# Kernel tuning notes

Hardware: AMD Instinct MI355X
Metric: run time of the kernel (lower is better)

Reference implementation:

```python
import jax, jax.numpy as jnp
import numpy as np

B, T, V, E_DIM, M_DIM, H = 32, 256, 10000, 300, 128, 256


def setup_inputs() -> dict:
    key = jax.random.key(0)
    ks = jax.random.split(key, 8)
    sc = 0.05
    words = jax.random.randint(ks[0], (B, T), 0, V)            # int token ids, 0 = pad
    midis = jax.random.normal(ks[1], (B, T, M_DIM), dtype=jnp.float32)
    E  = jax.random.normal(ks[2], (V, E_DIM), dtype=jnp.float32) * sc   # embedding table
    Wm = jax.random.normal(ks[3], (M_DIM, E_DIM), dtype=jnp.float32) * sc  # midi Dense
    bm = jnp.zeros((E_DIM,), jnp.float32)
    Wx = jax.random.normal(ks[4], (E_DIM, 3 * H), dtype=jnp.float32) * sc  # GRU input kernel [z|r|h]
    bx = jnp.zeros((3 * H,), jnp.float32)
    U  = jax.random.normal(ks[5], (H, 3 * H), dtype=jnp.float32) * sc      # GRU recurrent kernel
    bu = jnp.zeros((3 * H,), jnp.float32)                                  # recurrent bias (reset_after)
    Wo = jax.random.normal(ks[6], (H, V), dtype=jnp.float32) * sc          # output Dense
    bo = jnp.zeros((V,), jnp.float32)
    return {"words": words, "midis": midis, "E": E, "Wm": Wm, "bm": bm,
            "Wx": Wx, "bx": bx, "U": U, "bu": bu, "Wo": Wo, "bo": bo}


def _gru_masked(x, mask, Wx, bx, U, bu):
    """Keras GRU (reset_after=True) with mask carry-through. x: [B,T,E], mask: [B,T] bool."""
    gx = x @ Wx + bx                      # [B,T,3H] precomputed input gates
    gx_t = jnp.swapaxes(gx, 0, 1)         # [T,B,3H]
    m_t = mask.T                          # [T,B]
    h0 = jnp.zeros((x.shape[0], H), x.dtype)

    def step(h, inp):
        g, m = inp
        gh = h @ U + bu                   # [B,3H]
        xz, xr, xn = jnp.split(g, 3, axis=-1)
        hz, hr, hn = jnp.split(gh, 3, axis=-1)
        z = jax.nn.sigmoid(xz + hz)
        r = jax.nn.sigmoid(xr + hr)
        n = jnp.tanh(xn + r * hn)         # reset_after: r applied to recurrent projection
        h_new = z * h + (1.0 - z) * n
        h_new = jnp.where(m[:, None], h_new, h)  # masked step: carry state/output
        return h_new, h_new

    h_last, seq = jax.lax.scan(step, h0, (gx_t, m_t))
    return jnp.swapaxes(seq, 0, 1), h_last  # [B,T,H], [B,H]


def reference(words, midis, E, Wm, bm, Wx, bx, U, bu, Wo, bo):
    mask = words != 0                      # Embedding(mask_zero=True).compute_mask
    x = E[words] + (midis @ Wm + bm)       # [B,T,E] fused embedding + dense add
    seq, _ = _gru_masked(x, mask, Wx, bx, U, bu)
    return seq @ Wo + bo                   # [B,T,V] logits
```

## Files before the change

### kernel.cpp

```cpp
#include <hip/hip_runtime.h>
#include <hip/hip_fp16.h>

typedef unsigned short ushort_t;
typedef short bf16x8 __attribute__((ext_vector_type(8)));
typedef float f32x4 __attribute__((ext_vector_type(4)));
typedef _Float16 f16x8 __attribute__((ext_vector_type(8)));

#define B_SZ 32
#define T_SZ 256
#define V_SZ 10000
#define E_DIM 300
#define M_DIM 128
#define H_SZ 256

__device__ __forceinline__ ushort_t f2bf(float f) {
  unsigned u = __float_as_uint(f);
  unsigned r = u + 0x7fffu + ((u >> 16) & 1u);
  return (ushort_t)(r >> 16);
}

__global__ void k_cast_bf16(const float* __restrict__ in, ushort_t* __restrict__ out, int n) {
  int i = blockIdx.x * blockDim.x + threadIdx.x;
  if (i < n) out[i] = f2bf(in[i]);
}

template <int MODE>
__global__ void k_transpose_cast(const float* __restrict__ in, ushort_t* __restrict__ out,
                                 int R, int C, int Rp, int Cp) {
  __shared__ float tile[32][33];
  int c0 = blockIdx.x * 32, r0 = blockIdx.y * 32;
  int tx = threadIdx.x, ty = threadIdx.y;
#pragma unroll
  for (int i = 0; i < 32; i += 8) {
    int r = r0 + ty + i, c = c0 + tx;
    tile[ty + i][tx] = (r < R && c < C) ? in[(size_t)r * C + c] : 0.f;
  }
  __syncthreads();
#pragma unroll
  for (int i = 0; i < 32; i += 8) {
    int c = c0 + ty + i, r = r0 + tx;
    if (c < Cp && r < Rp) {
      float v = tile[tx][ty + i];
      if (MODE == 0) {
        out[(size_t)c * Rp + r] = f2bf(v);
      } else {
        __half h = __float2half(v);
        out[(size_t)c * Rp + r] = *(ushort_t*)&h;
      }
    }
  }
}

__global__ void k_xfuse(const float* __restrict__ xtmp, const float* __restrict__ E,
                        const int* __restrict__ words, ushort_t* __restrict__ xb) {
  int m = blockIdx.x;
  int kp = threadIdx.x;
  int w = words[m];
  float v = 0.f;
  if (kp < E_DIM) v = xtmp[(size_t)m * 320 + kp] + E[(size_t)w * E_DIM + kp];
  xb[(size_t)m * 320 + kp] = f2bf(v);
}

__global__ __launch_bounds__(256, 2) void k_gemm_bt(
    const ushort_t* __restrict__ A, const ushort_t* __restrict__ BT,
    const float* __restrict__ bias, float* __restrict__ C,
    int M, int K, int Nreal, int ldc) {
  __shared__ __align__(16) char smem[32768];
  char* As = smem;
  char* Bs = smem + 16384;
  const int tid = threadIdx.x;
  const int lane = tid & 63;
  const int w = tid >> 6;
  const int wr = w >> 1, wc = w & 1;
  const int m0 = blockIdx.x * 128;
  const int n0 = blockIdx.y * 128;

  f32x4 acc[4][4];
#pragma unroll
  for (int i = 0; i < 4; ++i)
#pragma unroll
    for (int j = 0; j < 4; ++j) acc[i][j] = (f32x4){0.f, 0.f, 0.f, 0.f};

  const int srow = tid >> 3;
  const int sc16 = tid & 7;

  for (int k0 = 0; k0 < K; k0 += 64) {
    __syncthreads();
#pragma unroll
    for (int it = 0; it < 4; ++it) {
      int row = srow + it * 32;
      int slot = sc16 ^ (row & 7);
      bf16x8 va = *(const bf16x8*)(A + (size_t)(m0 + row) * K + k0 + sc16 * 8);
      *(bf16x8*)(As + row * 128 + (slot << 4)) = va;
      bf16x8 vb = *(const bf16x8*)(BT + (size_t)(n0 + row) * K + k0 + sc16 * 8);
      *(bf16x8*)(Bs + row * 128 + (slot << 4)) = vb;
    }
    __syncthreads();

    bf16x8 af[4][2], bfr[4][2];
#pragma unroll
    for (int mi = 0; mi < 4; ++mi) {
      int r = wr * 64 + mi * 16 + (lane & 15);
#pragma unroll
      for (int kk = 0; kk < 2; ++kk) {
        int c16 = kk * 4 + (lane >> 4);
        af[mi][kk] = *(const bf16x8*)(As + r * 128 + ((c16 ^ (r & 7)) << 4));
      }
    }
#pragma unroll
    for (int ni = 0; ni < 4; ++ni) {
      int r = wc * 64 + ni * 16 + (lane & 15);
#pragma unroll
      for (int kk = 0; kk < 2; ++kk) {
        int c16 = kk * 4 + (lane >> 4);
        bfr[ni][kk] = *(const bf16x8*)(Bs + r * 128 + ((c16 ^ (r & 7)) << 4));
      }
    }
#pragma unroll
    for (int mi = 0; mi < 4; ++mi)
#pragma unroll
      for (int ni = 0; ni < 4; ++ni)
#pragma unroll
        for (int kk = 0; kk < 2; ++kk)
          acc[mi][ni] = __builtin_amdgcn_mfma_f32_16x16x32_bf16(af[mi][kk], bfr[ni][kk],
                                                                acc[mi][ni], 0, 0, 0);
  }

  const int rbase = m0 + wr * 64 + (lane >> 4) * 4;
  const int cbase = n0 + wc * 64 + (lane & 15);
#pragma unroll
  for (int ni = 0; ni < 4; ++ni) {
    int n = cbase + ni * 16;
    if (n < Nreal) {
      float bn = bias[n];
#pragma unroll
      for (int mi = 0; mi < 4; ++mi) {
#pragma unroll
        for (int rg = 0; rg < 4; ++rg) {
          int mrow = rbase + mi * 16 + rg;
          C[(size_t)mrow * ldc + n] = acc[mi][ni][rg] + bn;
        }
      }
    }
  }
}

__global__ __launch_bounds__(512, 2) void k_gru(
    const float* __restrict__ gx, const ushort_t* __restrict__ UT,
    const float* __restrict__ bu, const int* __restrict__ words,
    ushort_t* __restrict__ seqb) {
  const int b = blockIdx.x;
  const int tid = threadIdx.x;
  const int lane = tid & 63;
  const int w = tid >> 6;

  __shared__ __align__(16) _Float16 hlds[16 * 256];
  __shared__ float ghbuf[768];
  __shared__ int words_s[T_SZ];

  for (int i = tid; i < 16 * 256; i += 512) hlds[i] = (_Float16)0.f;
  if (tid < T_SZ) words_s[tid] = words[b * T_SZ + tid];

  f16x8 Ufrag[6][8];
  {
    const int n0 = w * 96;
    const ushort_t* src = UT + (size_t)(n0 + (lane & 15)) * 256 + (lane >> 4) * 8;
#pragma unroll
    for (int ni = 0; ni < 6; ++ni) {
#pragma unroll
      for (int kk = 0; kk < 8; ++kk)
        Ufrag[ni][kk] = *(const f16x8*)(src + (size_t)ni * 16 * 256 + kk * 32);
    }
  }
  float buz = 0.f, bur = 0.f, bun = 0.f;
  if (tid < H_SZ) {
    buz = bu[tid];
    bur = bu[H_SZ + tid];
    bun = bu[2 * H_SZ + tid];
  }
  __syncthreads();

  const float* gxp = gx + (size_t)b * T_SZ * 768;
  float gxz = 0.f, gxr = 0.f, gxn = 0.f;
  if (tid < H_SZ) {
    gxz = gxp[tid];
    gxr = gxp[H_SZ + tid];
    gxn = gxp[2 * H_SZ + tid];
  }
  float h_old = 0.f;

  const int arow = lane & 15;
  const int abase = arow * 512;
  const int asub = lane >> 4;
  const int aswz = arow & 7;

  for (int t = 0; t < T_SZ; ++t) {
    float gxz_n = 0.f, gxr_n = 0.f, gxn_n = 0.f;
    if (t + 1 < T_SZ && tid < H_SZ) {
      const float* g1 = gxp + (size_t)(t + 1) * 768;
      gxz_n = g1[tid];
      gxr_n = g1[H_SZ + tid];
      gxn_n = g1[2 * H_SZ + tid];
    }

    f32x4 acc[6];
#pragma unroll
    for (int ni = 0; ni < 6; ++ni) acc[ni] = (f32x4){0.f, 0.f, 0.f, 0.f};
#pragma unroll
    for (int kk = 0; kk < 8; ++kk) {
      int c = kk * 4 + asub;
      f16x8 afrag = *(const f16x8*)((const char*)hlds + abase + ((c ^ aswz) << 4));
#pragma unroll
      for (int ni = 0; ni < 6; ++ni)
        acc[ni] = __builtin_amdgcn_mfma_f32_16x16x32_f16(afrag, Ufrag[ni][kk], acc[ni], 0, 0, 0);
    }
    if (lane < 16) {
      const int nb = w * 96 + lane;
#pragma unroll
      for (int ni = 0; ni < 6; ++ni) ghbuf[nb + ni * 16] = acc[ni][0];
    }
    __syncthreads();

    if (tid < H_SZ) {
      float hz = ghbuf[tid] + buz;
      float hr = ghbuf[H_SZ + tid] + bur;
      float hn = ghbuf[2 * H_SZ + tid] + bun;
      float z = 1.f / (1.f + __expf(-(gxz + hz)));
      float r = 1.f / (1.f + __expf(-(gxr + hr)));
      float nv = 2.f / (1.f + __expf(-2.f * (gxn + r * hn))) - 1.f;
      float hnew = (words_s[t] != 0) ? (z * h_old + (1.f - z) * nv) : h_old;
      h_old = hnew;
      seqb[((size_t)b * T_SZ + t) * H_SZ + tid] = f2bf(hnew);
      hlds[tid] = (_Float16)hnew;
    }
    __syncthreads();
    gxz = gxz_n;
    gxr = gxr_n;
    gxn = gxn_n;
  }
}

extern "C" void kernel_launch(void* const* d_in, const int* in_sizes, int n_in,
                              void* d_out, int out_size, void* d_ws, size_t ws_size,
                              hipStream_t stream) {
  const int*   words = (const int*)d_in[0];
  const float* midis = (const float*)d_in[1];
  const float* E     = (const float*)d_in[2];
  const float* Wm    = (const float*)d_in[3];
  const float* bm    = (const float*)d_in[4];
  const float* Wx    = (const float*)d_in[5];
  const float* bx    = (const float*)d_in[6];
  const float* U     = (const float*)d_in[7];
  const float* bu    = (const float*)d_in[8];
  const float* Wo    = (const float*)d_in[9];
  const float* bo    = (const float*)d_in[10];
  float* out = (float*)d_out;

  const int MT = B_SZ * T_SZ;
  size_t off = 0;
  auto alloc = [&](size_t bytes) -> void* {
    void* p = (char*)d_ws + off;
    off += (bytes + 255) & ~(size_t)255;
    return p;
  };
  ushort_t* mid_b = (ushort_t*)alloc((size_t)MT * 128 * 2);
  ushort_t* WmT   = (ushort_t*)alloc((size_t)384 * 128 * 2);
  float*    xtmp  = (float*)   alloc((size_t)MT * 320 * 4);
  ushort_t* x_b   = (ushort_t*)alloc((size_t)MT * 320 * 2);
  ushort_t* WxT   = (ushort_t*)alloc((size_t)768 * 320 * 2);
  float*    gx    = (float*)   alloc((size_t)MT * 768 * 4);
  ushort_t* UT    = (ushort_t*)alloc((size_t)768 * 256 * 2);
  ushort_t* seq_b = (ushort_t*)alloc((size_t)MT * 256 * 2);
  ushort_t* WoT   = (ushort_t*)alloc((size_t)10112 * 256 * 2);
  (void)ws_size;

  k_cast_bf16<<<(MT * 128 + 255) / 256, 256, 0, stream>>>(midis, mid_b, MT * 128);
  k_transpose_cast<0><<<dim3(12, 4),  dim3(32, 8), 0, stream>>>(Wm, WmT, 128, 300, 128, 384);
  k_transpose_cast<0><<<dim3(24, 10), dim3(32, 8), 0, stream>>>(Wx, WxT, 300, 768, 320, 768);
  k_transpose_cast<0><<<dim3(316, 8), dim3(32, 8), 0, stream>>>(Wo, WoT, 256, 10000, 256, 10112);
  k_transpose_cast<1><<<dim3(24, 8),  dim3(32, 8), 0, stream>>>(U, UT, 256, 768, 256, 768);

  k_gemm_bt<<<dim3(64, 3), 256, 0, stream>>>(mid_b, WmT, bm, xtmp, MT, 128, 300, 320);
  k_xfuse<<<MT, 320, 0, stream>>>(xtmp, E, words, x_b);
  k_gemm_bt<<<dim3(64, 6), 256, 0, stream>>>(x_b, WxT, bx, gx, MT, 320, 768, 768);
  k_gru<<<B_SZ, 512, 0, stream>>>(gx, UT, bu, words, seq_b);
  k_gemm_bt<<<dim3(64, 79), 256, 0, stream>>>(seq_b, WoT, bo, out, MT, 256, 10000, 10000);
}
```

Before: 464.6 us.

## Halve GRU block to 256 threads with 12 MFMA tiles per wave

The recurrent GRU kernel now runs with 4 waves of 256 threads instead of 8 waves of 512. Each wave holds 12 U column tiles in registers, about 384 VGPRs of fragments, and every thread does the gate math, so no threads sit idle. The recurrent bias is folded into the MFMA accumulator init, and the bf16 store of h is deferred one step so it overlaps the next step's work. Each wave now issues twice as many serial MFMAs per step and register pressure rises sharply, which risks spills and a longer per-step critical path, traded against cheaper barriers.

```diff
diff --git a/kernel.cpp b/kernel.cpp
--- a/kernel.cpp
+++ b/kernel.cpp
@@ -145,7 +145,7 @@
   }
 }
 
-__global__ __launch_bounds__(512, 2) void k_gru(
+__global__ __launch_bounds__(256, 1) void k_gru(
     const float* __restrict__ gx, const ushort_t* __restrict__ UT,
     const float* __restrict__ bu, const int* __restrict__ words,
     ushort_t* __restrict__ seqb) {
@@ -158,36 +158,32 @@
   __shared__ float ghbuf[768];
   __shared__ int words_s[T_SZ];
 
-  for (int i = tid; i < 16 * 256; i += 512) hlds[i] = (_Float16)0.f;
-  if (tid < T_SZ) words_s[tid] = words[b * T_SZ + tid];
-
-  f16x8 Ufrag[6][8];
+  for (int i = tid; i < 16 * 256; i += 256) hlds[i] = (_Float16)0.f;
+  words_s[tid] = words[b * T_SZ + tid];
+
+  f16x8 Ufrag[12][8];
+  const int n0 = w * 192;
   {
-    const int n0 = w * 96;
     const ushort_t* src = UT + (size_t)(n0 + (lane & 15)) * 256 + (lane >> 4) * 8;
 #pragma unroll
-    for (int ni = 0; ni < 6; ++ni) {
+    for (int ni = 0; ni < 12; ++ni) {
 #pragma unroll
       for (int kk = 0; kk < 8; ++kk)
         Ufrag[ni][kk] = *(const f16x8*)(src + (size_t)ni * 16 * 256 + kk * 32);
     }
   }
-  float buz = 0.f, bur = 0.f, bun = 0.f;
-  if (tid < H_SZ) {
-    buz = bu[tid];
-    bur = bu[H_SZ + tid];
-    bun = bu[2 * H_SZ + tid];
-  }
+  float bub[12];
+#pragma unroll
+  for (int ni = 0; ni < 12; ++ni) bub[ni] = (lane < 16) ? bu[n0 + ni * 16 + lane] : 0.f;
+
   __syncthreads();
 
   const float* gxp = gx + (size_t)b * T_SZ * 768;
-  float gxz = 0.f, gxr = 0.f, gxn = 0.f;
-  if (tid < H_SZ) {
-    gxz = gxp[tid];
-    gxr = gxp[H_SZ + tid];
-    gxn = gxp[2 * H_SZ + tid];
-  }
+  float gxz = gxp[tid];
+  float gxr = gxp[H_SZ + tid];
+  float gxn = gxp[2 * H_SZ + tid];
   float h_old = 0.f;
+  float h_pend = 0.f;
 
   const int arow = lane & 15;
   const int abase = arow * 512;
@@ -195,49 +191,52 @@
   const int aswz = arow & 7;
 
   for (int t = 0; t < T_SZ; ++t) {
+    if (t > 0) seqb[((size_t)b * T_SZ + (t - 1)) * H_SZ + tid] = f2bf(h_pend);
+
     float gxz_n = 0.f, gxr_n = 0.f, gxn_n = 0.f;
-    if (t + 1 < T_SZ && tid < H_SZ) {
+    if (t + 1 < T_SZ) {
       const float* g1 = gxp + (size_t)(t + 1) * 768;
       gxz_n = g1[tid];
       gxr_n = g1[H_SZ + tid];
       gxn_n = g1[2 * H_SZ + tid];
     }
 
-    f32x4 acc[6];
-#pragma unroll
-    for (int ni = 0; ni < 6; ++ni) acc[ni] = (f32x4){0.f, 0.f, 0.f, 0.f};
+    f32x4 acc[12];
+#pragma unroll
+    for (int ni = 0; ni < 12; ++ni) acc[ni] = (f32x4){bub[ni], 0.f, 0.f, 0.f};
 #pragma unroll
     for (int kk = 0; kk < 8; ++kk) {
       int c = kk * 4 + asub;
       f16x8 afrag = *(const f16x8*)((const char*)hlds + abase + ((c ^ aswz) << 4));
 #pragma unroll
-      for (int ni = 0; ni < 6; ++ni)
+      for (int ni = 0; ni < 12; ++ni)
         acc[ni] = __builtin_amdgcn_mfma_f32_16x16x32_f16(afrag, Ufrag[ni][kk], acc[ni], 0, 0, 0);
     }
     if (lane < 16) {
-      const int nb = w * 96 + lane;
-#pragma unroll
-      for (int ni = 0; ni < 6; ++ni) ghbuf[nb + ni * 16] = acc[ni][0];
-    }
-    __syncthreads();
-
-    if (tid < H_SZ) {
-      float hz = ghbuf[tid] + buz;
-      float hr = ghbuf[H_SZ + tid] + bur;
-      float hn = ghbuf[2 * H_SZ + tid] + bun;
+#pragma unroll
+      for (int ni = 0; ni < 12; ++ni) ghbuf[n0 + ni * 16 + lane] = acc[ni][0];
+    }
+    __syncthreads();
+
+    {
+      float hz = ghbuf[tid];
+      float hr = ghbuf[H_SZ + tid];
+      float hn = ghbuf[2 * H_SZ + tid];
       float z = 1.f / (1.f + __expf(-(gxz + hz)));
       float r = 1.f / (1.f + __expf(-(gxr + hr)));
       float nv = 2.f / (1.f + __expf(-2.f * (gxn + r * hn))) - 1.f;
       float hnew = (words_s[t] != 0) ? (z * h_old + (1.f - z) * nv) : h_old;
       h_old = hnew;
-      seqb[((size_t)b * T_SZ + t) * H_SZ + tid] = f2bf(hnew);
+      h_pend = hnew;
       hlds[tid] = (_Float16)hnew;
     }
     __syncthreads();
+
     gxz = gxz_n;
     gxr = gxr_n;
     gxn = gxn_n;
   }
+  seqb[((size_t)b * T_SZ + (T_SZ - 1)) * H_SZ + tid] = f2bf(h_pend);
 }
 
 extern "C" void kernel_launch(void* const* d_in, const int* in_sizes, int n_in,
@@ -283,6 +282,6 @@
   k_gemm_bt<<<dim3(64, 3), 256, 0, stream>>>(mid_b, WmT, bm, xtmp, MT, 128, 300, 320);
   k_xfuse<<<MT, 320, 0, stream>>>(xtmp, E, words, x_b);
   k_gemm_bt<<<dim3(64, 6), 256, 0, stream>>>(x_b, WxT, bx, gx, MT, 320, 768, 768);
-  k_gru<<<B_SZ, 512, 0, stream>>>(gx, UT, bu, words, seq_b);
+  k_gru<<<B_SZ, 256, 0, stream>>>(gx, UT, bu, words, seq_b);
   k_gemm_bt<<<dim3(64, 79), 256, 0, stream>>>(seq_b, WoT, bo, out, MT, 256, 10000, 10000);
 }
```

New measurement: 677.8 us. 1.46x slower.

## Interleave two batch sequences per GRU block to overlap MFMA with gate math

Applied to the files above, without the earlier changes.

Each GRU block now runs two batch rows, staggered by half a step, so the recurrent MFMA for one sequence overlaps the sigmoid/tanh gate update of the other. Grid size halves to 16 blocks and U is loaded into registers once per pair of sequences. The recurrent bias is folded into the MFMA accumulator init, and the seq stores are deferred one phase. The cost is longer per-block serial work (two sequences per block) and more LDS and register use.

```diff
diff --git a/kernel.cpp b/kernel.cpp
--- a/kernel.cpp
+++ b/kernel.cpp
@@ -149,21 +149,31 @@
     const float* __restrict__ gx, const ushort_t* __restrict__ UT,
     const float* __restrict__ bu, const int* __restrict__ words,
     ushort_t* __restrict__ seqb) {
-  const int b = blockIdx.x;
+  const int bA = blockIdx.x * 2;
+  const int bB = bA + 1;
   const int tid = threadIdx.x;
   const int lane = tid & 63;
   const int w = tid >> 6;
 
-  __shared__ __align__(16) _Float16 hlds[16 * 256];
-  __shared__ float ghbuf[768];
-  __shared__ int words_s[T_SZ];
-
-  for (int i = tid; i < 16 * 256; i += 512) hlds[i] = (_Float16)0.f;
-  if (tid < T_SZ) words_s[tid] = words[b * T_SZ + tid];
+  __shared__ __align__(16) _Float16 hA[16 * 256];
+  __shared__ __align__(16) _Float16 hB[16 * 256];
+  __shared__ float ghA[768];
+  __shared__ float ghB[768];
+  __shared__ int wA_s[T_SZ];
+  __shared__ int wB_s[T_SZ];
+
+  for (int i = tid; i < 16 * 256; i += 512) {
+    hA[i] = (_Float16)0.f;
+    hB[i] = (_Float16)0.f;
+  }
+  if (tid < T_SZ) {
+    wA_s[tid] = words[bA * T_SZ + tid];
+    wB_s[tid] = words[bB * T_SZ + tid];
+  }
 
   f16x8 Ufrag[6][8];
+  const int n0 = w * 96;
   {
-    const int n0 = w * 96;
     const ushort_t* src = UT + (size_t)(n0 + (lane & 15)) * 256 + (lane >> 4) * 8;
 #pragma unroll
     for (int ni = 0; ni < 6; ++ni) {
@@ -172,22 +182,21 @@
         Ufrag[ni][kk] = *(const f16x8*)(src + (size_t)ni * 16 * 256 + kk * 32);
     }
   }
-  float buz = 0.f, bur = 0.f, bun = 0.f;
+  float bub[6];
+#pragma unroll
+  for (int ni = 0; ni < 6; ++ni) bub[ni] = (lane < 16) ? bu[n0 + ni * 16 + lane] : 0.f;
+
+  __syncthreads();
+
+  const float* gxA = gx + (size_t)bA * T_SZ * 768;
+  const float* gxB = gx + (size_t)bB * T_SZ * 768;
+  float gAz = 0.f, gAr = 0.f, gAn = 0.f, gBz = 0.f, gBr = 0.f, gBn = 0.f;
   if (tid < H_SZ) {
-    buz = bu[tid];
-    bur = bu[H_SZ + tid];
-    bun = bu[2 * H_SZ + tid];
-  }
-  __syncthreads();
-
-  const float* gxp = gx + (size_t)b * T_SZ * 768;
-  float gxz = 0.f, gxr = 0.f, gxn = 0.f;
-  if (tid < H_SZ) {
-    gxz = gxp[tid];
-    gxr = gxp[H_SZ + tid];
-    gxn = gxp[2 * H_SZ + tid];
-  }
-  float h_old = 0.f;
+    gAz = gxA[tid];
+    gAr = gxA[H_SZ + tid];
+    gAn = gxA[2 * H_SZ + tid];
+  }
+  float hOldA = 0.f, hOldB = 0.f, pendA = 0.f, pendB = 0.f;
 
   const int arow = lane & 15;
   const int abase = arow * 512;
@@ -195,48 +204,104 @@
   const int aswz = arow & 7;
 
   for (int t = 0; t < T_SZ; ++t) {
-    float gxz_n = 0.f, gxr_n = 0.f, gxn_n = 0.f;
-    if (t + 1 < T_SZ && tid < H_SZ) {
-      const float* g1 = gxp + (size_t)(t + 1) * 768;
-      gxz_n = g1[tid];
-      gxr_n = g1[H_SZ + tid];
-      gxn_n = g1[2 * H_SZ + tid];
+    if (t > 0 && tid < H_SZ)
+      seqb[((size_t)bA * T_SZ + (t - 1)) * H_SZ + tid] = f2bf(pendA);
+
+    float gAz_n = 0.f, gAr_n = 0.f, gAn_n = 0.f, gBz_n = 0.f, gBr_n = 0.f, gBn_n = 0.f;
+    if (tid < H_SZ) {
+      if (t + 1 < T_SZ) {
+        const float* g1 = gxA + (size_t)(t + 1) * 768;
+        gAz_n = g1[tid];
+        gAr_n = g1[H_SZ + tid];
+        gAn_n = g1[2 * H_SZ + tid];
+      }
+      const float* g2 = gxB + (size_t)t * 768;
+      gBz_n = g2[tid];
+      gBr_n = g2[H_SZ + tid];
+      gBn_n = g2[2 * H_SZ + tid];
     }
 
     f32x4 acc[6];
 #pragma unroll
-    for (int ni = 0; ni < 6; ++ni) acc[ni] = (f32x4){0.f, 0.f, 0.f, 0.f};
+    for (int ni = 0; ni < 6; ++ni) acc[ni] = (f32x4){bub[ni], 0.f, 0.f, 0.f};
 #pragma unroll
     for (int kk = 0; kk < 8; ++kk) {
       int c = kk * 4 + asub;
-      f16x8 afrag = *(const f16x8*)((const char*)hlds + abase + ((c ^ aswz) << 4));
+      f16x8 afrag = *(const f16x8*)((const char*)hA + abase + ((c ^ aswz) << 4));
 #pragma unroll
       for (int ni = 0; ni < 6; ++ni)
         acc[ni] = __builtin_amdgcn_mfma_f32_16x16x32_f16(afrag, Ufrag[ni][kk], acc[ni], 0, 0, 0);
     }
+
+    if (t > 0 && tid < H_SZ) {
+      float hz = ghB[tid];
+      float hr = ghB[H_SZ + tid];
+      float hn = ghB[2 * H_SZ + tid];
+      float z = 1.f / (1.f + __expf(-(gBz + hz)));
+      float r = 1.f / (1.f + __expf(-(gBr + hr)));
+      float nv = 2.f / (1.f + __expf(-2.f * (gBn + r * hn))) - 1.f;
+      float hnew = (wB_s[t - 1] != 0) ? (z * hOldB + (1.f - z) * nv) : hOldB;
+      hOldB = hnew;
+      pendB = hnew;
+      hB[tid] = (_Float16)hnew;
+    }
     if (lane < 16) {
-      const int nb = w * 96 + lane;
-#pragma unroll
-      for (int ni = 0; ni < 6; ++ni) ghbuf[nb + ni * 16] = acc[ni][0];
+#pragma unroll
+      for (int ni = 0; ni < 6; ++ni) ghA[n0 + ni * 16 + lane] = acc[ni][0];
     }
     __syncthreads();
 
+    if (t > 0 && tid < H_SZ)
+      seqb[((size_t)bB * T_SZ + (t - 1)) * H_SZ + tid] = f2bf(pendB);
+
+    f32x4 acc2[6];
+#pragma unroll
+    for (int ni = 0; ni < 6; ++ni) acc2[ni] = (f32x4){bub[ni], 0.f, 0.f, 0.f};
+#pragma unroll
+    for (int kk = 0; kk < 8; ++kk) {
+      int c = kk * 4 + asub;
+      f16x8 afrag = *(const f16x8*)((const char*)hB + abase + ((c ^ aswz) << 4));
+#pragma unroll
+      for (int ni = 0; ni < 6; ++ni)
+        acc2[ni] = __builtin_amdgcn_mfma_f32_16x16x32_f16(afrag, Ufrag[ni][kk], acc2[ni], 0, 0, 0);
+    }
+
     if (tid < H_SZ) {
-      float hz = ghbuf[tid] + buz;
-      float hr = ghbuf[H_SZ + tid] + bur;
-      float hn = ghbuf[2 * H_SZ + tid] + bun;
-      float z = 1.f / (1.f + __expf(-(gxz + hz)));
-      float r = 1.f / (1.f + __expf(-(gxr + hr)));
-      float nv = 2.f / (1.f + __expf(-2.f * (gxn + r * hn))) - 1.f;
-      float hnew = (words_s[t] != 0) ? (z * h_old + (1.f - z) * nv) : h_old;
-      h_old = hnew;
-      seqb[((size_t)b * T_SZ + t) * H_SZ + tid] = f2bf(hnew);
-      hlds[tid] = (_Float16)hnew;
+      float hz = ghA[tid];
+      float hr = ghA[H_SZ + tid];
+      float hn = ghA[2 * H_SZ + tid];
+      float z = 1.f / (1.f + __expf(-(gAz + hz)));
+      float r = 1.f / (1.f + __expf(-(gAr + hr)));
+      float nv = 2.f / (1.f + __expf(-2.f * (gAn + r * hn))) - 1.f;
+      float hnew = (wA_s[t] != 0) ? (z * hOldA + (1.f - z) * nv) : hOldA;
+      hOldA = hnew;
+      pendA = hnew;
+      hA[tid] = (_Float16)hnew;
+    }
+    if (lane < 16) {
+#pragma unroll
+      for (int ni = 0; ni < 6; ++ni) ghB[n0 + ni * 16 + lane] = acc2[ni][0];
     }
     __syncthreads();
-    gxz = gxz_n;
-    gxr = gxr_n;
-    gxn = gxn_n;
+
+    gAz = gAz_n;
+    gAr = gAr_n;
+    gAn = gAn_n;
+    gBz = gBz_n;
+    gBr = gBr_n;
+    gBn = gBn_n;
+  }
+
+  if (tid < H_SZ) {
+    seqb[((size_t)bA * T_SZ + (T_SZ - 1)) * H_SZ + tid] = f2bf(pendA);
+    float hz = ghB[tid];
+    float hr = ghB[H_SZ + tid];
+    float hn = ghB[2 * H_SZ + tid];
+    float z = 1.f / (1.f + __expf(-(gBz + hz)));
+    float r = 1.f / (1.f + __expf(-(gBr + hr)));
+    float nv = 2.f / (1.f + __expf(-2.f * (gBn + r * hn))) - 1.f;
+    float hnew = (wB_s[T_SZ - 1] != 0) ? (z * hOldB + (1.f - z) * nv) : hOldB;
+    seqb[((size_t)bB * T_SZ + (T_SZ - 1)) * H_SZ + tid] = f2bf(hnew);
   }
 }
 
@@ -283,6 +348,6 @@
   k_gemm_bt<<<dim3(64, 3), 256, 0, stream>>>(mid_b, WmT, bm, xtmp, MT, 128, 300, 320);
   k_xfuse<<<MT, 320, 0, stream>>>(xtmp, E, words, x_b);
   k_gemm_bt<<<dim3(64, 6), 256, 0, stream>>>(x_b, WxT, bx, gx, MT, 320, 768, 768);
-  k_gru<<<B_SZ, 512, 0, stream>>>(gx, UT, bu, words, seq_b);
+  k_gru<<<B_SZ / 2, 512, 0, stream>>>(gx, UT, bu, words, seq_b);
   k_gemm_bt<<<dim3(64, 79), 256, 0, stream>>>(seq_b, WoT, bo, out, MT, 256, 10000, 10000);
 }
```

Measured after the change: 1.393 ms. 3x slower.
